# Optimization experiments

Hardware: AMD Instinct MI355X
Metric: run time of the kernel (lower is better)

Reference implementation:

```python
import jax, jax.numpy as jnp
import numpy as np

N_NODES = 100000
N_EDGES = 1000000
DIM = 128
N_RELS = 500
N_TIMES = 1000


def setup_inputs() -> dict:
    key = jax.random.key(0)
    ks = jax.random.split(key, 8)
    h = jax.random.normal(ks[0], (N_NODES, DIM), dtype=jnp.float32)
    edge_index = jax.random.randint(ks[1], (2, N_EDGES), 0, N_NODES, dtype=jnp.int64)
    edge_type = jax.random.randint(ks[2], (N_EDGES,), 0, N_RELS, dtype=jnp.int64)
    edge_time = jax.random.randint(ks[3], (N_EDGES,), 0, N_TIMES, dtype=jnp.int64)
    query_rel = 7
    rel_table = jax.random.normal(ks[4], (N_RELS, DIM), dtype=jnp.float32)
    time_table = jax.random.normal(ks[5], (N_TIMES, DIM), dtype=jnp.float32)
    # Linear weights stored as [in, out] so y = x @ W + b
    W1 = jax.random.normal(ks[6], (4 * DIM, DIM), dtype=jnp.float32) * (1.0 / np.sqrt(4 * DIM))
    b1 = jnp.zeros((DIM,), dtype=jnp.float32)
    W2 = jax.random.normal(ks[7], (DIM, 1), dtype=jnp.float32) * (1.0 / np.sqrt(DIM))
    b2 = jnp.zeros((1,), dtype=jnp.float32)
    return {"h": h, "edge_index": edge_index, "edge_type": edge_type,
            "edge_time": edge_time, "query_rel": query_rel,
            "rel_table": rel_table, "time_table": time_table,
            "W1": W1, "b1": b1, "W2": W2, "b2": b2}


def reference(h, edge_index, edge_type, edge_time, query_rel,
              rel_table, time_table, W1, b1, W2, b2):
    src = edge_index[0]                    # [E]
    h_s = h[src]                           # [E, D] gather
    h_r = rel_table[edge_type]             # [E, D] embedding lookup
    h_t = time_table[edge_time]            # [E, D] embedding lookup
    h_rq = jnp.broadcast_to(rel_table[query_rel][None, :], h_s.shape)  # [E, D]
    x = jnp.concatenate([h_s, h_r, h_rq, h_t], axis=1)  # [E, 4D]
    hidden = jax.nn.relu(x @ W1 + b1)      # [E, D]
    alpha = hidden @ W2 + b2               # [E, 1]
    return jax.nn.sigmoid(alpha)[:, 0]     # [E]
```

## Files before the change

kernel.cpp:

```cpp
#include <hip/hip_runtime.h>
#include <hip/hip_fp16.h>
#include <math.h>

#define DIM 128

typedef _Float16 half8 __attribute__((ext_vector_type(8)));
typedef float floatx4 __attribute__((ext_vector_type(4)));

__global__ __launch_bounds__(256) void precompute(
    const float* __restrict__ h, const float* __restrict__ rel,
    const float* __restrict__ tim, const int* __restrict__ qrel,
    const float* __restrict__ W1, const float* __restrict__ b1,
    __half* __restrict__ Hh, __half* __restrict__ Rh, __half* __restrict__ Th,
    int n_nodes, int n_rels, int n_times, int nHB, int nRB)
{
    const int tid = threadIdx.x;
    const int b = blockIdx.x;

    const float* A; __half* Out; int M, k0, row0; bool isR = false;
    if (b < nHB)            { A = h;   Out = Hh; M = n_nodes; k0 = 0;   row0 = b * 64; }
    else if (b < nHB + nRB) { A = rel; Out = Rh; M = n_rels;  k0 = 128; row0 = (b - nHB) * 64; isR = true; }
    else                    { A = tim; Out = Th; M = n_times; k0 = 384; row0 = (b - nHB - nRB) * 64; }

    __shared__ _Float16 fragB[32 * 64 * 8];
    __shared__ float c0f[DIM];

    for (int idx = tid; idx < DIM * DIM; idx += 256) {
        const int k = idx >> 7, n = idx & 127;
        const float v = W1[(size_t)(k0 + k) * DIM + n];
        const int ct = n >> 4, n15 = n & 15;
        const int kc = k >> 5, kr = k & 31, q = kr >> 3, j = kr & 7;
        fragB[(((ct * 4 + kc) * 64) + (q * 16 + n15)) * 8 + j] = (_Float16)v;
    }
    if (isR && tid < DIM) {
        const int q = qrel[0];
        const float* hq = rel + (size_t)q * DIM;
        float s = b1[tid];
        for (int k = 0; k < DIM; ++k)
            s = fmaf(hq[k], W1[(size_t)(256 + k) * DIM + tid], s);
        c0f[tid] = s;
    }
    __syncthreads();

    const int w = tid >> 6;
    const int lane = tid & 63;
    const int m15 = lane & 15, q = lane >> 4;

    int arow = row0 + w * 16 + m15;
    if (arow >= M) arow = M - 1;
    const float* aBase = A + (size_t)arow * DIM + q * 8;

    floatx4 acc[8];
#pragma unroll
    for (int ct = 0; ct < 8; ++ct) acc[ct] = (floatx4)0.f;

#pragma unroll
    for (int kc = 0; kc < 4; ++kc) {
        const float4 a0 = *(const float4*)(aBase + kc * 32);
        const float4 a1 = *(const float4*)(aBase + kc * 32 + 4);
        half8 af;
        af[0] = (_Float16)a0.x; af[1] = (_Float16)a0.y;
        af[2] = (_Float16)a0.z; af[3] = (_Float16)a0.w;
        af[4] = (_Float16)a1.x; af[5] = (_Float16)a1.y;
        af[6] = (_Float16)a1.z; af[7] = (_Float16)a1.w;
#pragma unroll
        for (int ct = 0; ct < 8; ++ct) {
            const half8 bf = *(half8*)&fragB[(((ct * 4 + kc) * 64) + lane) * 8];
            acc[ct] = __builtin_amdgcn_mfma_f32_16x16x32_f16(af, bf, acc[ct], 0, 0, 0);
        }
    }

#pragma unroll
    for (int ct = 0; ct < 8; ++ct) {
        const int col = ct * 16 + m15;
        const float cadd = isR ? c0f[col] : 0.f;
#pragma unroll
        for (int r = 0; r < 4; ++r) {
            const int m = row0 + w * 16 + q * 4 + r;
            if (m < M)
                Out[(size_t)m * DIM + col] = (_Float16)(acc[ct][r] + cadd);
        }
    }
}

__device__ __forceinline__ float dot8(uint4 hu, uint4 ru, uint4 tu,
                                      float4 wA, float4 wB) {
    union U { uint4 u; __half2 h[4]; };
    U hv, rv, tv; hv.u = hu; rv.u = ru; tv.u = tu;
    const float w[8] = {wA.x, wA.y, wA.z, wA.w, wB.x, wB.y, wB.z, wB.w};
    float p = 0.f;
#pragma unroll
    for (int j = 0; j < 4; ++j) {
        const __half2 s = __hadd2(__hadd2(hv.h[j], rv.h[j]), tv.h[j]);
        const float2 f = __half22float2(s);
        p = fmaf(fmaxf(f.x, 0.f), w[2 * j], p);
        p = fmaf(fmaxf(f.y, 0.f), w[2 * j + 1], p);
    }
    return p;
}

__global__ __launch_bounds__(256) void edge_kernel(
    const int* __restrict__ ei, const int* __restrict__ ety,
    const int* __restrict__ eti,
    const __half* __restrict__ Hh, const __half* __restrict__ Rh,
    const __half* __restrict__ Th,
    const float* __restrict__ W2, const float* __restrict__ b2,
    float* __restrict__ out, int E, int nGrpTotal)
{
    const int tid = threadIdx.x;
    const int l = tid & 15;
    int g = blockIdx.x * 16 + (tid >> 4);
    const int nPair = E >> 1;
    if (g >= nPair) return;

    const float4 wA = ((const float4*)W2)[2 * l];
    const float4 wB = ((const float4*)W2)[2 * l + 1];
    const float b2v = b2[0];

    int s0 = ei[2 * g],  s1 = ei[2 * g + 1];
    int r0 = ety[2 * g], r1 = ety[2 * g + 1];
    int t0 = eti[2 * g], t1 = eti[2 * g + 1];

    while (true) {
        const int gn = g + nGrpTotal;
        const uint4 hv0 = ((const uint4*)(Hh + (size_t)s0 * DIM))[l];
        const uint4 rv0 = ((const uint4*)(Rh + (size_t)r0 * DIM))[l];
        const uint4 tv0 = ((const uint4*)(Th + (size_t)t0 * DIM))[l];
        const uint4 hv1 = ((const uint4*)(Hh + (size_t)s1 * DIM))[l];
        const uint4 rv1 = ((const uint4*)(Rh + (size_t)r1 * DIM))[l];
        const uint4 tv1 = ((const uint4*)(Th + (size_t)t1 * DIM))[l];
        if (gn < nPair) {
            s0 = ei[2 * gn];  s1 = ei[2 * gn + 1];
            r0 = ety[2 * gn]; r1 = ety[2 * gn + 1];
            t0 = eti[2 * gn]; t1 = eti[2 * gn + 1];
        }
        float p0 = dot8(hv0, rv0, tv0, wA, wB);
        float p1 = dot8(hv1, rv1, tv1, wA, wB);
#pragma unroll
        for (int off = 8; off > 0; off >>= 1) {
            p0 += __shfl_down(p0, off, 16);
            p1 += __shfl_down(p1, off, 16);
        }
        if (l == 0) {
            out[2 * g]     = 1.f / (1.f + __expf(-(p0 + b2v)));
            out[2 * g + 1] = 1.f / (1.f + __expf(-(p1 + b2v)));
        }
        if (gn >= nPair) break;
        g = gn;
    }
}

extern "C" void kernel_launch(void* const* d_in, const int* in_sizes, int n_in,
                              void* d_out, int out_size, void* d_ws, size_t ws_size,
                              hipStream_t stream) {
    const float* h          = (const float*)d_in[0];
    const int*   edge_index = (const int*)d_in[1];
    const int*   edge_type  = (const int*)d_in[2];
    const int*   edge_time  = (const int*)d_in[3];
    const int*   query_rel  = (const int*)d_in[4];
    const float* rel_table  = (const float*)d_in[5];
    const float* time_table = (const float*)d_in[6];
    const float* W1         = (const float*)d_in[7];
    const float* b1         = (const float*)d_in[8];
    const float* W2         = (const float*)d_in[9];
    const float* b2         = (const float*)d_in[10];
    float* out = (float*)d_out;

    const int n_nodes = in_sizes[0] / DIM;
    const int E       = in_sizes[2];
    const int n_rels  = in_sizes[5] / DIM;
    const int n_times = in_sizes[6] / DIM;

    __half* Hh = (__half*)d_ws;
    __half* Rh = Hh + (size_t)n_nodes * DIM;
    __half* Th = Rh + (size_t)n_rels * DIM;

    const int nHB = (n_nodes + 63) / 64;
    const int nRB = (n_rels + 63) / 64;
    const int nTB = (n_times + 63) / 64;

    precompute<<<nHB + nRB + nTB, 256, 0, stream>>>(
        h, rel_table, time_table, query_rel, W1, b1,
        Hh, Rh, Th, n_nodes, n_rels, n_times, nHB, nRB);

    const int nBlk = 2048;
    edge_kernel<<<nBlk, 256, 0, stream>>>(
        edge_index, edge_type, edge_time, Hh, Rh, Th, W2, b2,
        out, E, nBlk * 16);
}
```

Baseline: 174.9 us.

## Double precompute rows per block and process four edges per group

The precompute kernel now handles 128 rows per block, with each wave computing two 16-row M tiles that share B fragments, and loads W1 as float4. This halves the W1 staging work per output row. The edge kernel processes four edges per 16-lane group instead of two, giving more gathers in flight per wave, and uses packed half relu with fdot2 against half-converted W2. Outputs are written as float4. The trade-offs are higher register pressure and W2 rounded to fp16.

```diff
diff --git a/kernel.cpp b/kernel.cpp
--- a/kernel.cpp
+++ b/kernel.cpp
@@ -5,6 +5,7 @@
 #define DIM 128
 
 typedef _Float16 half8 __attribute__((ext_vector_type(8)));
+typedef _Float16 half2v __attribute__((ext_vector_type(2)));
 typedef float floatx4 __attribute__((ext_vector_type(4)));
 
 __global__ __launch_bounds__(256) void precompute(
@@ -18,19 +19,24 @@
     const int b = blockIdx.x;
 
     const float* A; __half* Out; int M, k0, row0; bool isR = false;
-    if (b < nHB)            { A = h;   Out = Hh; M = n_nodes; k0 = 0;   row0 = b * 64; }
-    else if (b < nHB + nRB) { A = rel; Out = Rh; M = n_rels;  k0 = 128; row0 = (b - nHB) * 64; isR = true; }
-    else                    { A = tim; Out = Th; M = n_times; k0 = 384; row0 = (b - nHB - nRB) * 64; }
+    if (b < nHB)            { A = h;   Out = Hh; M = n_nodes; k0 = 0;   row0 = b * 128; }
+    else if (b < nHB + nRB) { A = rel; Out = Rh; M = n_rels;  k0 = 128; row0 = (b - nHB) * 128; isR = true; }
+    else                    { A = tim; Out = Th; M = n_times; k0 = 384; row0 = (b - nHB - nRB) * 128; }
 
     __shared__ _Float16 fragB[32 * 64 * 8];
     __shared__ float c0f[DIM];
 
-    for (int idx = tid; idx < DIM * DIM; idx += 256) {
-        const int k = idx >> 7, n = idx & 127;
-        const float v = W1[(size_t)(k0 + k) * DIM + n];
-        const int ct = n >> 4, n15 = n & 15;
+    for (int idx4 = tid; idx4 < DIM * DIM / 4; idx4 += 256) {
+        const int k = idx4 >> 5;
+        const int n0 = (idx4 & 31) * 4;
+        const float4 v = *(const float4*)&W1[(size_t)(k0 + k) * DIM + n0];
         const int kc = k >> 5, kr = k & 31, q = kr >> 3, j = kr & 7;
-        fragB[(((ct * 4 + kc) * 64) + (q * 16 + n15)) * 8 + j] = (_Float16)v;
+        const float vv[4] = {v.x, v.y, v.z, v.w};
+#pragma unroll
+        for (int i = 0; i < 4; ++i) {
+            const int n = n0 + i, ct = n >> 4, n15 = n & 15;
+            fragB[(((ct * 4 + kc) * 64) + (q * 16 + n15)) * 8 + j] = (_Float16)vv[i];
+        }
     }
     if (isR && tid < DIM) {
         const int q = qrel[0];
@@ -46,55 +52,71 @@
     const int lane = tid & 63;
     const int m15 = lane & 15, q = lane >> 4;
 
-    int arow = row0 + w * 16 + m15;
-    if (arow >= M) arow = M - 1;
-    const float* aBase = A + (size_t)arow * DIM + q * 8;
-
-    floatx4 acc[8];
-#pragma unroll
-    for (int ct = 0; ct < 8; ++ct) acc[ct] = (floatx4)0.f;
+    const float* aBase[2];
+#pragma unroll
+    for (int mt = 0; mt < 2; ++mt) {
+        int arow = row0 + w * 32 + mt * 16 + m15;
+        if (arow >= M) arow = M - 1;
+        aBase[mt] = A + (size_t)arow * DIM + q * 8;
+    }
+
+    floatx4 acc[2][8];
+#pragma unroll
+    for (int mt = 0; mt < 2; ++mt)
+#pragma unroll
+        for (int ct = 0; ct < 8; ++ct) acc[mt][ct] = (floatx4)0.f;
 
 #pragma unroll
     for (int kc = 0; kc < 4; ++kc) {
-        const float4 a0 = *(const float4*)(aBase + kc * 32);
-        const float4 a1 = *(const float4*)(aBase + kc * 32 + 4);
-        half8 af;
-        af[0] = (_Float16)a0.x; af[1] = (_Float16)a0.y;
-        af[2] = (_Float16)a0.z; af[3] = (_Float16)a0.w;
-        af[4] = (_Float16)a1.x; af[5] = (_Float16)a1.y;
-        af[6] = (_Float16)a1.z; af[7] = (_Float16)a1.w;
+        half8 af[2];
+#pragma unroll
+        for (int mt = 0; mt < 2; ++mt) {
+            const float4 a0 = *(const float4*)(aBase[mt] + kc * 32);
+            const float4 a1 = *(const float4*)(aBase[mt] + kc * 32 + 4);
+            af[mt][0] = (_Float16)a0.x; af[mt][1] = (_Float16)a0.y;
+            af[mt][2] = (_Float16)a0.z; af[mt][3] = (_Float16)a0.w;
+            af[mt][4] = (_Float16)a1.x; af[mt][5] = (_Float16)a1.y;
+            af[mt][6] = (_Float16)a1.z; af[mt][7] = (_Float16)a1.w;
+        }
 #pragma unroll
         for (int ct = 0; ct < 8; ++ct) {
             const half8 bf = *(half8*)&fragB[(((ct * 4 + kc) * 64) + lane) * 8];
-            acc[ct] = __builtin_amdgcn_mfma_f32_16x16x32_f16(af, bf, acc[ct], 0, 0, 0);
-        }
-    }
-
-#pragma unroll
-    for (int ct = 0; ct < 8; ++ct) {
-        const int col = ct * 16 + m15;
-        const float cadd = isR ? c0f[col] : 0.f;
-#pragma unroll
-        for (int r = 0; r < 4; ++r) {
-            const int m = row0 + w * 16 + q * 4 + r;
-            if (m < M)
-                Out[(size_t)m * DIM + col] = (_Float16)(acc[ct][r] + cadd);
-        }
-    }
-}
-
-__device__ __forceinline__ float dot8(uint4 hu, uint4 ru, uint4 tu,
-                                      float4 wA, float4 wB) {
-    union U { uint4 u; __half2 h[4]; };
-    U hv, rv, tv; hv.u = hu; rv.u = ru; tv.u = tu;
-    const float w[8] = {wA.x, wA.y, wA.z, wA.w, wB.x, wB.y, wB.z, wB.w};
+            acc[0][ct] = __builtin_amdgcn_mfma_f32_16x16x32_f16(af[0], bf, acc[0][ct], 0, 0, 0);
+            acc[1][ct] = __builtin_amdgcn_mfma_f32_16x16x32_f16(af[1], bf, acc[1][ct], 0, 0, 0);
+        }
+    }
+
+#pragma unroll
+    for (int mt = 0; mt < 2; ++mt)
+#pragma unroll
+        for (int ct = 0; ct < 8; ++ct) {
+            const int col = ct * 16 + m15;
+            const float cadd = isR ? c0f[col] : 0.f;
+#pragma unroll
+            for (int r = 0; r < 4; ++r) {
+                const int m = row0 + w * 32 + mt * 16 + q * 4 + r;
+                if (m < M)
+                    Out[(size_t)m * DIM + col] = (_Float16)(acc[mt][ct][r] + cadd);
+            }
+        }
+}
+
+__device__ __forceinline__ float edot(uint4 hu, uint4 ru, uint4 tu,
+                                      const half2v* __restrict__ w2h) {
+    union U { uint4 u; half2v h[4]; };
+    U H, R, T; H.u = hu; R.u = ru; T.u = tu;
+    const half2v z = (half2v)(_Float16)0.f;
     float p = 0.f;
 #pragma unroll
     for (int j = 0; j < 4; ++j) {
-        const __half2 s = __hadd2(__hadd2(hv.h[j], rv.h[j]), tv.h[j]);
-        const float2 f = __half22float2(s);
-        p = fmaf(fmaxf(f.x, 0.f), w[2 * j], p);
-        p = fmaf(fmaxf(f.y, 0.f), w[2 * j + 1], p);
+        half2v s = H.h[j] + R.h[j] + T.h[j];
+        s = __builtin_elementwise_max(s, z);
+#if __has_builtin(__builtin_amdgcn_fdot2)
+        p = __builtin_amdgcn_fdot2(s, w2h[j], p, false);
+#else
+        p = fmaf((float)s[0], (float)w2h[j][0], p);
+        p = fmaf((float)s[1], (float)w2h[j][1], p);
+#endif
     }
     return p;
 }
@@ -110,42 +132,66 @@
     const int tid = threadIdx.x;
     const int l = tid & 15;
     int g = blockIdx.x * 16 + (tid >> 4);
-    const int nPair = E >> 1;
-    if (g >= nPair) return;
+    const int nQuad = (E + 3) >> 2;
+    if (g >= nQuad) return;
 
     const float4 wA = ((const float4*)W2)[2 * l];
     const float4 wB = ((const float4*)W2)[2 * l + 1];
+    half2v w2h[4];
+    w2h[0][0] = (_Float16)wA.x; w2h[0][1] = (_Float16)wA.y;
+    w2h[1][0] = (_Float16)wA.z; w2h[1][1] = (_Float16)wA.w;
+    w2h[2][0] = (_Float16)wB.x; w2h[2][1] = (_Float16)wB.y;
+    w2h[3][0] = (_Float16)wB.z; w2h[3][1] = (_Float16)wB.w;
     const float b2v = b2[0];
 
-    int s0 = ei[2 * g],  s1 = ei[2 * g + 1];
-    int r0 = ety[2 * g], r1 = ety[2 * g + 1];
-    int t0 = eti[2 * g], t1 = eti[2 * g + 1];
+    int s[4], r[4], t[4];
+#pragma unroll
+    for (int i = 0; i < 4; ++i) {
+        const int e = min(4 * g + i, E - 1);
+        s[i] = ei[e]; r[i] = ety[e]; t[i] = eti[e];
+    }
 
     while (true) {
         const int gn = g + nGrpTotal;
-        const uint4 hv0 = ((const uint4*)(Hh + (size_t)s0 * DIM))[l];
-        const uint4 rv0 = ((const uint4*)(Rh + (size_t)r0 * DIM))[l];
-        const uint4 tv0 = ((const uint4*)(Th + (size_t)t0 * DIM))[l];
-        const uint4 hv1 = ((const uint4*)(Hh + (size_t)s1 * DIM))[l];
-        const uint4 rv1 = ((const uint4*)(Rh + (size_t)r1 * DIM))[l];
-        const uint4 tv1 = ((const uint4*)(Th + (size_t)t1 * DIM))[l];
-        if (gn < nPair) {
-            s0 = ei[2 * gn];  s1 = ei[2 * gn + 1];
-            r0 = ety[2 * gn]; r1 = ety[2 * gn + 1];
-            t0 = eti[2 * gn]; t1 = eti[2 * gn + 1];
-        }
-        float p0 = dot8(hv0, rv0, tv0, wA, wB);
-        float p1 = dot8(hv1, rv1, tv1, wA, wB);
+        uint4 hv[4], rv[4], tv[4];
+#pragma unroll
+        for (int i = 0; i < 4; ++i) {
+            hv[i] = ((const uint4*)(Hh + (size_t)s[i] * DIM))[l];
+            rv[i] = ((const uint4*)(Rh + (size_t)r[i] * DIM))[l];
+            tv[i] = ((const uint4*)(Th + (size_t)t[i] * DIM))[l];
+        }
+        if (gn < nQuad) {
+#pragma unroll
+            for (int i = 0; i < 4; ++i) {
+                const int e = min(4 * gn + i, E - 1);
+                s[i] = ei[e]; r[i] = ety[e]; t[i] = eti[e];
+            }
+        }
+        float p[4];
+#pragma unroll
+        for (int i = 0; i < 4; ++i)
+            p[i] = edot(hv[i], rv[i], tv[i], w2h);
 #pragma unroll
         for (int off = 8; off > 0; off >>= 1) {
-            p0 += __shfl_down(p0, off, 16);
-            p1 += __shfl_down(p1, off, 16);
+#pragma unroll
+            for (int i = 0; i < 4; ++i)
+                p[i] += __shfl_down(p[i], off, 16);
         }
         if (l == 0) {
-            out[2 * g]     = 1.f / (1.f + __expf(-(p0 + b2v)));
-            out[2 * g + 1] = 1.f / (1.f + __expf(-(p1 + b2v)));
-        }
-        if (gn >= nPair) break;
+            const int e0 = 4 * g;
+            float4 o;
+            o.x = 1.f / (1.f + __expf(-(p[0] + b2v)));
+            o.y = 1.f / (1.f + __expf(-(p[1] + b2v)));
+            o.z = 1.f / (1.f + __expf(-(p[2] + b2v)));
+            o.w = 1.f / (1.f + __expf(-(p[3] + b2v)));
+            if (e0 + 3 < E) {
+                *(float4*)(out + e0) = o;
+            } else {
+                const float ov[4] = {o.x, o.y, o.z, o.w};
+                for (int i = 0; i < 4 && e0 + i < E; ++i) out[e0 + i] = ov[i];
+            }
+        }
+        if (gn >= nQuad) break;
         g = gn;
     }
 }
@@ -175,9 +221,9 @@
     __half* Rh = Hh + (size_t)n_nodes * DIM;
     __half* Th = Rh + (size_t)n_rels * DIM;
 
-    const int nHB = (n_nodes + 63) / 64;
-    const int nRB = (n_rels + 63) / 64;
-    const int nTB = (n_times + 63) / 64;
+    const int nHB = (n_nodes + 127) / 128;
+    const int nRB = (n_rels + 127) / 128;
+    const int nTB = (n_times + 127) / 128;
 
     precompute<<<nHB + nRB + nTB, 256, 0, stream>>>(
         h, rel_table, time_table, query_rel, W1, b1,
```

New measurement: 179.7 us. +2.8%, slower.
